# Kernel optimization log

Hardware: AMD Instinct MI355X
Metric: run time of the kernel (lower is better)

The kernel has to match this reference:

```python
import jax, jax.numpy as jnp
import numpy as np
import math

B, S, H = 2, 4096, 512
NUM_HEADS = 8
HEAD_DIM = H // NUM_HEADS
RECENCY_DECAY = 0.9


def setup_inputs() -> dict:
    key = jax.random.key(0)
    k1, k2, k3 = jax.random.split(key, 3)
    scale = 1.0 / math.sqrt(H)
    x = jax.random.normal(k1, (B, S, H), dtype=jnp.float32)
    w_qkv = jax.random.normal(k2, (3 * H, H), dtype=jnp.float32) * scale
    w_out = jax.random.normal(k3, (H, H), dtype=jnp.float32) * scale
    b_out = jnp.zeros((H,), dtype=jnp.float32)
    return {"x": x, "w_qkv": w_qkv, "w_out": w_out, "b_out": b_out}


def reference(x, w_qkv, w_out, b_out):
    batch, seq_len, hidden = x.shape
    nh, hd = NUM_HEADS, HEAD_DIM
    # qkv projection (no bias): torch Linear computes x @ W.T
    qkv = jnp.einsum('bsh,oh->bso', x, w_qkv)
    qkv = qkv.reshape(batch, seq_len, 3, nh, hd)
    q, k, v = jnp.transpose(qkv, (2, 0, 3, 1, 4))  # each [B, nh, S, hd]
    attn = jnp.einsum('bhqd,bhkd->bhqk', q, k) / math.sqrt(hd)
    # recency bias: positions[i, j] = j - i; bias = (j-i)*log(decay) for j<=i else 0
    pos = jnp.arange(seq_len)[None, :] - jnp.arange(seq_len)[:, None]
    bias = jnp.where(pos <= 0, pos.astype(jnp.float32) * math.log(RECENCY_DECAY),
                     jnp.zeros((), dtype=jnp.float32))
    attn = jax.nn.softmax(attn + bias[None, None, :, :], axis=-1)
    out = jnp.einsum('bhqk,bhkd->bqhd', attn, v).reshape(batch, seq_len, hidden)
    return jnp.einsum('bsh,oh->bso', out, w_out) + b_out
```

## Files before the change

kernel.cpp:

```cpp
#include <hip/hip_runtime.h>
#include <hip/hip_bf16.h>
#include <stdint.h>

#define B_   2
#define S_   4096
#define H_   512
#define NH_  8
#define HD_  64
#define M_   (B_*S_)
#define LOG2D (-0.15200309344504997f)
#define SC2   (0.18033688011112042f)

#define NFULL        4
#define NCHUNK       16

typedef __attribute__((ext_vector_type(8))) short bf16x8_t;
typedef __attribute__((ext_vector_type(4))) float f32x4_t;

__device__ __forceinline__ void gl_lds16(const __hip_bfloat16* g, __hip_bfloat16* l) {
  __builtin_amdgcn_global_load_lds(
      (__attribute__((address_space(1))) void*)(g),
      (__attribute__((address_space(3))) void*)(l),
      16, 0, 0);
}

__global__ __launch_bounds__(256)
void cast3_kernel(const float* __restrict__ x, const float* __restrict__ wq,
                  const float* __restrict__ wo,
                  __hip_bfloat16* __restrict__ xb, __hip_bfloat16* __restrict__ wqb,
                  __hip_bfloat16* __restrict__ wob) {
  const int N0 = M_ * H_;
  const int N1 = 3 * H_ * H_;
  int i4 = (blockIdx.x * blockDim.x + threadIdx.x) * 4;
  const float* src; __hip_bfloat16* dst; int off;
  if (i4 < N0)           { src = x;  dst = xb;  off = i4; }
  else if (i4 < N0 + N1) { src = wq; dst = wqb; off = i4 - N0; }
  else                   { src = wo; dst = wob; off = i4 - N0 - N1; }
  float4 v = *(const float4*)(src + off);
  ushort4 o;
  __hip_bfloat16 h;
  h = __float2bfloat16(v.x); o.x = *(unsigned short*)&h;
  h = __float2bfloat16(v.y); o.y = *(unsigned short*)&h;
  h = __float2bfloat16(v.z); o.z = *(unsigned short*)&h;
  h = __float2bfloat16(v.w); o.w = *(unsigned short*)&h;
  *(ushort4*)((unsigned short*)dst + off) = o;
}

template<int EPI>
__global__ __launch_bounds__(256)
void gemm_bt(const __hip_bfloat16* __restrict__ A,
             const __hip_bfloat16* __restrict__ Bw,
             int K,
             __hip_bfloat16* __restrict__ qb,
             __hip_bfloat16* __restrict__ kb,
             __hip_bfloat16* __restrict__ vtb,
             float* __restrict__ outp,
             const float* __restrict__ bias) {
  __shared__ alignas(16) __hip_bfloat16 sA[128*64];
  __shared__ alignas(16) __hip_bfloat16 sB[128*64];
  const int tid  = threadIdx.x;
  const int wave = tid >> 6, lane = tid & 63;
  const int quad = lane >> 4, l15 = lane & 15;
  const int wr = (wave >> 1) * 64, wc = (wave & 1) * 64;
  const int m0 = blockIdx.y * 128, n0 = blockIdx.x * 128;

  const int sub  = lane >> 3;
  const int plog = (lane & 7) ^ sub;

  f32x4_t acc[4][4] = {};

  for (int kt = 0; kt < K; kt += 64) {
    __syncthreads();
    #pragma unroll
    for (int cc = 0; cc < 4; cc++) {
      int c   = wave * 4 + cc;
      int row = c * 8 + sub;
      gl_lds16(A  + (size_t)(m0 + row) * K + kt + plog * 8, sA + c * 512);
      gl_lds16(Bw + (size_t)(n0 + row) * K + kt + plog * 8, sB + c * 512);
    }
    __syncthreads();
    #pragma unroll
    for (int kh = 0; kh < 2; kh++) {
      bf16x8_t af[4], bfr[4];
      #pragma unroll
      for (int x = 0; x < 4; x++) {
        int row = wr + x * 16 + l15;
        int pos = kh * 4 + quad;
        af[x] = *(const bf16x8_t*)(sA + row * 64 + ((pos ^ (row & 7)) << 3));
      }
      #pragma unroll
      for (int y = 0; y < 4; y++) {
        int row = wc + y * 16 + l15;
        int pos = kh * 4 + quad;
        bfr[y] = *(const bf16x8_t*)(sB + row * 64 + ((pos ^ (row & 7)) << 3));
      }
      #pragma unroll
      for (int x = 0; x < 4; x++)
        #pragma unroll
        for (int y = 0; y < 4; y++)
          acc[x][y] = __builtin_amdgcn_mfma_f32_16x16x32_bf16(af[x], bfr[y], acc[x][y], 0, 0, 0);
    }
  }

  if (EPI == 0 && (n0 >> 9) == 2) {
    #pragma unroll
    for (int x = 0; x < 4; x++) {
      int gr = m0 + wr + x * 16 + quad * 4;
      int bb = gr >> 12, sb = gr & 4095;
      #pragma unroll
      for (int y = 0; y < 4; y++) {
        int rem = (n0 - 1024) + wc + y * 16 + l15;
        int h = rem >> 6, d = rem & 63;
        ushort4 o; __hip_bfloat16 hv;
        hv = __float2bfloat16(acc[x][y][0]); o.x = *(unsigned short*)&hv;
        hv = __float2bfloat16(acc[x][y][1]); o.y = *(unsigned short*)&hv;
        hv = __float2bfloat16(acc[x][y][2]); o.z = *(unsigned short*)&hv;
        hv = __float2bfloat16(acc[x][y][3]); o.w = *(unsigned short*)&hv;
        *(ushort4*)(vtb + ((size_t)(bb * NH_ + h) * HD_ + d) * S_ + sb) = o;
      }
    }
  } else {
    #pragma unroll
    for (int x = 0; x < 4; x++) {
      #pragma unroll
      for (int y = 0; y < 4; y++) {
        #pragma unroll
        for (int r = 0; r < 4; r++) {
          int gr = m0 + wr + x*16 + quad*4 + r;
          int gc = n0 + wc + y*16 + l15;
          float v = acc[x][y][r];
          if (EPI == 0) {
            int bb = gr >> 12, s = gr & 4095;
            int t  = gc >> 9,  rem = gc & 511;
            int h  = rem >> 6, d = rem & 63;
            __hip_bfloat16 hv = __float2bfloat16(v);
            int bh = bb * NH_ + h;
            if (t == 0) qb[((size_t)bh * S_ + s) * HD_ + d] = hv;
            else        kb[((size_t)bh * S_ + s) * HD_ + d] = hv;
          } else {
            outp[(size_t)gr * H_ + gc] = v + bias[gc];
          }
        }
      }
    }
  }
}

__device__ __forceinline__ void stage_kv(const __hip_bfloat16* __restrict__ kb,
                                         const __hip_bfloat16* __restrict__ vtb,
                                         int bh, int j0,
                                         __hip_bfloat16* dK, __hip_bfloat16* dV,
                                         int wave, int lane, int sub, int plog) {
  if (wave < 2) {
    #pragma unroll
    for (int cc = 0; cc < 4; cc++) {
      int c = wave * 4 + cc;
      gl_lds16(kb + ((size_t)bh * S_ + j0 + c * 8 + sub) * HD_ + plog * 8, dK + c * 512);
    }
  } else {
    #pragma unroll
    for (int cc = 0; cc < 4; cc++) {
      int c = (wave - 2) * 4 + cc;
      gl_lds16(vtb + ((size_t)bh * HD_ + c * 8 + sub) * S_ + j0 + plog * 8, dV + c * 512);
    }
  }
}

__global__ __launch_bounds__(256)
void attn_kernel(const __hip_bfloat16* __restrict__ qb,
                 const __hip_bfloat16* __restrict__ kb,
                 const __hip_bfloat16* __restrict__ vtb,
                 __hip_bfloat16* __restrict__ ob,
                 float* __restrict__ pO,
                 float* __restrict__ pl) {
  __shared__ alignas(16) __hip_bfloat16 sK[2][64*64];
  __shared__ alignas(16) __hip_bfloat16 sV[2][64*64];
  __shared__ alignas(16) __hip_bfloat16 sP[4][16*64];

  const int tid  = threadIdx.x;
  const int wave = tid >> 6, lane = tid & 63;
  const int quad = lane >> 4, l15 = lane & 15;
  const int w  = blockIdx.x;
  const int bh = blockIdx.y;

  int q0, jt0, chunk = 0;
  bool direct;
  if (w < 60) { q0 = 256 + w * 64; jt0 = 0; direct = true; }
  else { int t = w - 60; chunk = t & 15; q0 = (t >> 4) * 64; jt0 = chunk * 4; direct = false; }

  const __hip_bfloat16* qrow = qb + ((size_t)bh * S_ + q0 + wave * 16 + l15) * HD_;
  bf16x8_t aQ0 = *(const bf16x8_t*)(qrow + quad * 8);
  bf16x8_t aQ1 = *(const bf16x8_t*)(qrow + 32 + quad * 8);

  f32x4_t accO[4] = {};
  float l_r[4], negM2[4];
  const int row_i = q0 + wave * 16 + quad * 4;
  #pragma unroll
  for (int r = 0; r < 4; r++) {
    l_r[r] = 0.f;
    negM2[r] = -(17.312340f - LOG2D * (float)(row_i + r));
  }

  const int sub  = lane >> 3;
  const int plog = (lane & 7) ^ sub;
  __hip_bfloat16* sPw = &sP[wave][0];

  stage_kv(kb, vtb, bh, jt0 * 64, &sK[0][0], &sV[0][0], wave, lane, sub, plog);

  for (int it = 0; it < 4; ++it) {
    const int cur = it & 1;
    __syncthreads();
    if (it < 3)
      stage_kv(kb, vtb, bh, (jt0 + it + 1) * 64,
               &sK[1 - cur][0], &sV[1 - cur][0], wave, lane, sub, plog);
    const __hip_bfloat16* cK = &sK[cur][0];
    const __hip_bfloat16* cV = &sV[cur][0];
    const int j0 = (jt0 + it) * 64;

    f32x4_t sfr[4];
    #pragma unroll
    for (int ni = 0; ni < 4; ni++) {
      int row = ni * 16 + l15;
      f32x4_t a = {};
      bf16x8_t b0 = *(const bf16x8_t*)(cK + row * 64 + ((quad       ^ (row & 7)) << 3));
      bf16x8_t b1 = *(const bf16x8_t*)(cK + row * 64 + (((quad + 4) ^ (row & 7)) << 3));
      a = __builtin_amdgcn_mfma_f32_16x16x32_bf16(aQ0, b0, a, 0, 0, 0);
      a = __builtin_amdgcn_mfma_f32_16x16x32_bf16(aQ1, b1, a, 0, 0, 0);
      sfr[ni] = a;
    }

    #pragma unroll
    for (int r = 0; r < 4; r++) {
      const float d0 = (float)(j0 + l15 - (row_i + r));
      const int row = quad * 4 + r;
      float psum = 0.f;
      #pragma unroll
      for (int ni = 0; ni < 4; ni++) {
        float dij = d0 + (float)(ni * 16);
        float arg = fmaf(fminf(dij, 0.f), LOG2D, fmaf(sfr[ni][r], SC2, negM2[r]));
        float p = __builtin_amdgcn_exp2f(arg);
        psum += p;
        int col = ni * 16 + l15;
        sPw[row * 64 + (((col >> 3) ^ (row & 7)) << 3) + (col & 7)] = __float2bfloat16(p);
      }
      l_r[r] += psum;
    }
    __builtin_amdgcn_sched_barrier(0);
    __builtin_amdgcn_s_waitcnt(0xC07F);
    __builtin_amdgcn_sched_barrier(0);

    bf16x8_t aP0 = *(const bf16x8_t*)(sPw + l15 * 64 + ((quad       ^ (l15 & 7)) << 3));
    bf16x8_t aP1 = *(const bf16x8_t*)(sPw + l15 * 64 + (((quad + 4) ^ (l15 & 7)) << 3));
    #pragma unroll
    for (int nd = 0; nd < 4; nd++) {
      int row = nd * 16 + l15;
      bf16x8_t b0 = *(const bf16x8_t*)(cV + row * 64 + ((quad       ^ (row & 7)) << 3));
      bf16x8_t b1 = *(const bf16x8_t*)(cV + row * 64 + (((quad + 4) ^ (row & 7)) << 3));
      accO[nd] = __builtin_amdgcn_mfma_f32_16x16x32_bf16(aP0, b0, accO[nd], 0, 0, 0);
      accO[nd] = __builtin_amdgcn_mfma_f32_16x16x32_bf16(aP1, b1, accO[nd], 0, 0, 0);
    }
    __builtin_amdgcn_sched_barrier(0);
  }

  #pragma unroll
  for (int r = 0; r < 4; r++) {
    float l = l_r[r];
    #pragma unroll
    for (int msk = 1; msk < 16; msk <<= 1) l += __shfl_xor(l, msk, 64);
    l_r[r] = l;
  }

  if (direct) {
    const int b = bh >> 3, h = bh & 7;
    #pragma unroll
    for (int r = 0; r < 4; r++) {
      float invr = 1.0f / l_r[r];
      #pragma unroll
      for (int nd = 0; nd < 4; nd++) {
        int srow = q0 + wave * 16 + quad * 4 + r;
        int col  = h * HD_ + nd * 16 + l15;
        ob[((size_t)b * S_ + srow) * H_ + col] = __float2bfloat16(accO[nd][r] * invr);
      }
    }
  } else {
    const int qt = q0 >> 6;
    size_t base = ((size_t)bh * NFULL + qt) * NCHUNK + chunk;
    float* po = pO + base * 4096;
    #pragma unroll
    for (int nd = 0; nd < 4; nd++)
      #pragma unroll
      for (int r = 0; r < 4; r++)
        po[(wave*16 + quad*4 + r) * 64 + nd*16 + l15] = accO[nd][r];
    if (l15 == 0) {
      #pragma unroll
      for (int r = 0; r < 4; r++)
        pl[base * 64 + wave*16 + quad*4 + r] = l_r[r];
    }
  }
}

__global__ __launch_bounds__(256)
void combine_kernel(const float* __restrict__ pO,
                    const float* __restrict__ pl,
                    __hip_bfloat16* __restrict__ ob) {
  const int f  = blockIdx.x;
  const int bh = blockIdx.y;
  const int tid = threadIdx.x;
  const int rr = tid >> 2, cg = (tid & 3) * 16;
  const size_t base0 = ((size_t)bh * NFULL + f) * NCHUNK;

  float L = 0.f;
  #pragma unroll
  for (int c = 0; c < NCHUNK; c++) L += pl[(base0 + c) * 64 + rr];
  const float inv = 1.0f / L;

  float o[16];
  #pragma unroll
  for (int k = 0; k < 16; k++) o[k] = 0.f;
  #pragma unroll
  for (int c = 0; c < NCHUNK; c++) {
    const float4* src = (const float4*)(pO + (base0 + c) * 4096 + rr * 64 + cg);
    #pragma unroll
    for (int k4 = 0; k4 < 4; k4++) {
      float4 v = src[k4];
      o[k4*4+0] += v.x; o[k4*4+1] += v.y;
      o[k4*4+2] += v.z; o[k4*4+3] += v.w;
    }
  }
  const int b = bh >> 3, h = bh & 7, s = f * 64 + rr;
  __hip_bfloat16* dst = ob + ((size_t)b * S_ + s) * H_ + h * HD_ + cg;
  #pragma unroll
  for (int k = 0; k < 16; k++) dst[k] = __float2bfloat16(o[k] * inv);
}

extern "C" void kernel_launch(void* const* d_in, const int* in_sizes, int n_in,
                              void* d_out, int out_size, void* d_ws, size_t ws_size,
                              hipStream_t stream) {
  const float* x     = (const float*)d_in[0];
  const float* w_qkv = (const float*)d_in[1];
  const float* w_out = (const float*)d_in[2];
  const float* b_out = (const float*)d_in[3];
  float* out = (float*)d_out;

  char* ws = (char*)d_ws;
  __hip_bfloat16* xb  = (__hip_bfloat16*)(ws);
  __hip_bfloat16* wqb = (__hip_bfloat16*)(ws + (8u  << 20));
  __hip_bfloat16* wob = (__hip_bfloat16*)(ws + (10u << 20));
  __hip_bfloat16* qb  = (__hip_bfloat16*)(ws + (11u << 20));
  __hip_bfloat16* kb  = (__hip_bfloat16*)(ws + (19u << 20));
  __hip_bfloat16* vtb = (__hip_bfloat16*)(ws + (27u << 20));
  float*          pO  = (float*)(ws + (36u << 20));
  float*          pl  = (float*)(ws + (53u << 20));
  __hip_bfloat16* ab  = xb;

  cast3_kernel<<<dim3(5120), dim3(256), 0, stream>>>(x, w_qkv, w_out, xb, wqb, wob);
  gemm_bt<0><<<dim3(12, 64), dim3(256), 0, stream>>>(xb, wqb, H_, qb, kb, vtb, nullptr, nullptr);
  attn_kernel<<<dim3(60 + NFULL * NCHUNK, B_ * NH_), dim3(256), 0, stream>>>(qb, kb, vtb, ab, pO, pl);
  combine_kernel<<<dim3(NFULL, B_ * NH_), dim3(256), 0, stream>>>(pO, pl, ab);
  gemm_bt<1><<<dim3(4, 64), dim3(256), 0, stream>>>(ab, wob, H_, nullptr, nullptr, nullptr, out, b_out);
}
```

Measured before the change: 140.6 us.

## Halve split-K chunks, store partial outputs in fp16, swizzle GEMM blocks per XCD

The attention split for the first query tiles now uses 8 KV chunks of 8 tiles each instead of 16 chunks of 4. The partial output buffers are stored as fp16 instead of fp32, which halves partial-sum traffic in both the attention and combine kernels. The GEMM remaps block indices so that each XCD gets a contiguous band of rows, aiming for better L2 reuse. This risks longer per-block work for the split blocks (load imbalance) and lower precision in the partial sums.

Measured after the change: 136.7 us. -2.8%, faster.

```diff
diff --git a/kernel.cpp b/kernel.cpp
--- a/kernel.cpp
+++ b/kernel.cpp
@@ -1,5 +1,6 @@
 #include <hip/hip_runtime.h>
 #include <hip/hip_bf16.h>
+#include <hip/hip_fp16.h>
 #include <stdint.h>
 
 #define B_   2
@@ -12,7 +13,7 @@
 #define SC2   (0.18033688011112042f)
 
 #define NFULL        4
-#define NCHUNK       16
+#define NCHUNK       8
 
 typedef __attribute__((ext_vector_type(8))) short bf16x8_t;
 typedef __attribute__((ext_vector_type(4))) float f32x4_t;
@@ -62,7 +63,14 @@
   const int wave = tid >> 6, lane = tid & 63;
   const int quad = lane >> 4, l15 = lane & 15;
   const int wr = (wave >> 1) * 64, wc = (wave & 1) * 64;
-  const int m0 = blockIdx.y * 128, n0 = blockIdx.x * 128;
+
+  const int nbx  = gridDim.x;
+  const int flat = blockIdx.y * nbx + blockIdx.x;
+  const int xcd  = flat & 7, sq = flat >> 3;
+  const int rows_per_xcd = gridDim.y >> 3;
+  const int by = xcd * rows_per_xcd + sq / nbx;
+  const int bx = sq % nbx;
+  const int m0 = by * 128, n0 = bx * 128;
 
   const int sub  = lane >> 3;
   const int plog = (lane & 7) ^ sub;
@@ -171,7 +179,7 @@
                  const __hip_bfloat16* __restrict__ kb,
                  const __hip_bfloat16* __restrict__ vtb,
                  __hip_bfloat16* __restrict__ ob,
-                 float* __restrict__ pO,
+                 __half* __restrict__ pO,
                  float* __restrict__ pl) {
   __shared__ alignas(16) __hip_bfloat16 sK[2][64*64];
   __shared__ alignas(16) __hip_bfloat16 sV[2][64*64];
@@ -183,10 +191,10 @@
   const int w  = blockIdx.x;
   const int bh = blockIdx.y;
 
-  int q0, jt0, chunk = 0;
+  int q0, jt0, niter, chunk = 0;
   bool direct;
-  if (w < 60) { q0 = 256 + w * 64; jt0 = 0; direct = true; }
-  else { int t = w - 60; chunk = t & 15; q0 = (t >> 4) * 64; jt0 = chunk * 4; direct = false; }
+  if (w < 60) { q0 = 256 + w * 64; jt0 = 0; niter = 4; direct = true; }
+  else { int t = w - 60; chunk = t & 7; q0 = (t >> 3) * 64; jt0 = chunk * 8; niter = 8; direct = false; }
 
   const __hip_bfloat16* qrow = qb + ((size_t)bh * S_ + q0 + wave * 16 + l15) * HD_;
   bf16x8_t aQ0 = *(const bf16x8_t*)(qrow + quad * 8);
@@ -207,10 +215,10 @@
 
   stage_kv(kb, vtb, bh, jt0 * 64, &sK[0][0], &sV[0][0], wave, lane, sub, plog);
 
-  for (int it = 0; it < 4; ++it) {
+  for (int it = 0; it < niter; ++it) {
     const int cur = it & 1;
     __syncthreads();
-    if (it < 3)
+    if (it < niter - 1)
       stage_kv(kb, vtb, bh, (jt0 + it + 1) * 64,
                &sK[1 - cur][0], &sV[1 - cur][0], wave, lane, sub, plog);
     const __hip_bfloat16* cK = &sK[cur][0];
@@ -285,12 +293,12 @@
   } else {
     const int qt = q0 >> 6;
     size_t base = ((size_t)bh * NFULL + qt) * NCHUNK + chunk;
-    float* po = pO + base * 4096;
+    __half* po = pO + base * 4096;
     #pragma unroll
     for (int nd = 0; nd < 4; nd++)
       #pragma unroll
       for (int r = 0; r < 4; r++)
-        po[(wave*16 + quad*4 + r) * 64 + nd*16 + l15] = accO[nd][r];
+        po[(wave*16 + quad*4 + r) * 64 + nd*16 + l15] = __float2half(accO[nd][r]);
     if (l15 == 0) {
       #pragma unroll
       for (int r = 0; r < 4; r++)
@@ -300,7 +308,7 @@
 }
 
 __global__ __launch_bounds__(256)
-void combine_kernel(const float* __restrict__ pO,
+void combine_kernel(const __half* __restrict__ pO,
                     const float* __restrict__ pl,
                     __hip_bfloat16* __restrict__ ob) {
   const int f  = blockIdx.x;
@@ -319,13 +327,9 @@
   for (int k = 0; k < 16; k++) o[k] = 0.f;
   #pragma unroll
   for (int c = 0; c < NCHUNK; c++) {
-    const float4* src = (const float4*)(pO + (base0 + c) * 4096 + rr * 64 + cg);
-    #pragma unroll
-    for (int k4 = 0; k4 < 4; k4++) {
-      float4 v = src[k4];
-      o[k4*4+0] += v.x; o[k4*4+1] += v.y;
-      o[k4*4+2] += v.z; o[k4*4+3] += v.w;
-    }
+    const __half* src = pO + (base0 + c) * 4096 + rr * 64 + cg;
+    #pragma unroll
+    for (int k = 0; k < 16; k++) o[k] += __half2float(src[k]);
   }
   const int b = bh >> 3, h = bh & 7, s = f * 64 + rr;
   __hip_bfloat16* dst = ob + ((size_t)b * S_ + s) * H_ + h * HD_ + cg;
@@ -349,8 +353,8 @@
   __hip_bfloat16* qb  = (__hip_bfloat16*)(ws + (11u << 20));
   __hip_bfloat16* kb  = (__hip_bfloat16*)(ws + (19u << 20));
   __hip_bfloat16* vtb = (__hip_bfloat16*)(ws + (27u << 20));
-  float*          pO  = (float*)(ws + (36u << 20));
-  float*          pl  = (float*)(ws + (53u << 20));
+  __half*         pO  = (__half*)(ws + (36u << 20));
+  float*          pl  = (float*)(ws + (41u << 20));
   __hip_bfloat16* ab  = xb;
 
   cast3_kernel<<<dim3(5120), dim3(256), 0, stream>>>(x, w_qkv, w_out, xb, wqb, wob);
```
